# Kernel optimization log

Hardware: AMD Instinct MI355X
Metric: run time of the kernel (lower is better)

The kernel has to match this reference:

```python
import math
import jax, jax.numpy as jnp
import numpy as np

DRAGON_ITERATIONS = 12
DRAGON_SMOOTHING = 0.1


def _dragon_patterns(iterations=DRAGON_ITERATIONS, smoothing=DRAGON_SMOOTHING):
    """Deterministic (non-learned) Dragon curve patterns, matching torch impl."""
    patterns = [np.array([0.5], dtype=np.float32)]
    kernel = np.ones(3, dtype=np.float32) / 3.0
    for _ in range(1, iterations):
        prev = patterns[-1]
        n = len(prev)
        newp = np.zeros(2 * n + 1, dtype=np.float32)
        newp[:n] = prev
        newp[n] = 0.5
        newp[n + 1:] = 1.0 - prev[::-1]
        if smoothing > 0:
            # conv1d with kernel_size=3, padding=1 (zero pad) == np.convolve 'same'
            newp = np.convolve(newp, kernel, mode='same').astype(np.float32)
        newp = (newp - newp.min()) / (newp.max() - newp.min() + 1e-8)
        patterns.append(newp.astype(np.float32))
    return patterns

_PATTERNS = _dragon_patterns()


def _interp_pattern(seq_len):
    """Linearly interpolate selected dragon pattern to seq_len (static shapes)."""
    it = min(int(math.log2(seq_len)), DRAGON_ITERATIONS - 1)
    pattern = _PATTERNS[it]
    if len(pattern) == seq_len:
        w = pattern.copy()
    else:
        x_old = np.linspace(0.0, 1.0, len(pattern), dtype=np.float64)
        x_new = np.linspace(0.0, 1.0, seq_len, dtype=np.float64)
        w = np.interp(x_new, x_old, pattern.astype(np.float64)).astype(np.float32)
    return it, jnp.asarray(w)


def setup_inputs() -> dict:
    key = jax.random.key(0)
    ks = jax.random.split(key, 8)
    B, S, D = 8, 2048, 512
    query = jax.random.normal(ks[0], (B, S, D), dtype=jnp.float32)
    k = jax.random.normal(ks[1], (B, S, D), dtype=jnp.float32)
    value = jax.random.normal(ks[2], (B, S, D), dtype=jnp.float32)
    pattern_scale = jnp.ones((DRAGON_ITERATIONS,), dtype=jnp.float32)
    pattern_bias = jnp.zeros((DRAGON_ITERATIONS,), dtype=jnp.float32)
    w1 = jax.random.normal(ks[3], (DRAGON_ITERATIONS, 64), dtype=jnp.float32) * (1.0 / math.sqrt(DRAGON_ITERATIONS))
    b1 = jnp.zeros((64,), dtype=jnp.float32)
    w2 = jax.random.normal(ks[4], (64, 1), dtype=jnp.float32) * (1.0 / 8.0)
    b2 = jnp.zeros((1,), dtype=jnp.float32)
    return {"query": query, "key": k, "value": value,
            "pattern_scale": pattern_scale, "pattern_bias": pattern_bias,
            "w1": w1, "b1": b1, "w2": w2, "b2": b2}


def reference(query, key, value, pattern_scale, pattern_bias, w1, b1, w2, b2):
    B, S, D = key.shape
    it, base_w = _interp_pattern(S)
    # learned affine + softplus on dragon weights
    dragon_w = jax.nn.softplus(base_w * pattern_scale[it] + pattern_bias[it])  # [S]
    weighted_keys = key * dragon_w[None, :, None]                              # [B,S,D]
    scores = jnp.einsum('bqd,bkd->bqk', query, weighted_keys) / math.sqrt(D)   # [B,S,S]
    attn = jax.nn.softmax(scores, axis=-1)
    # blend factor from one-hot iteration features through tiny MLP
    feat = jax.nn.one_hot(it, DRAGON_ITERATIONS, dtype=query.dtype)            # [12]
    h = jax.nn.relu(feat @ w1 + b1)
    blend = jax.nn.sigmoid(h @ w2 + b2)                                        # [1]
    blend = blend[0]
    final_attn = blend * attn + (1.0 - blend) / S                              # uniform blend
    out = jnp.einsum('bqk,bkd->bqd', final_attn, value)                        # [B,S,D]
    # original does output.squeeze(1); S>1 so it's a no-op here
    return out
```

## Files before the change

### kernel.cpp

```cpp
#include <hip/hip_runtime.h>
#include <cstdint>

#define DEV __device__ __forceinline__

typedef float f32x4 __attribute__((ext_vector_type(4)));
typedef short s16x8 __attribute__((ext_vector_type(8)));

DEV unsigned short f2bf(float f){
    unsigned u = __builtin_bit_cast(unsigned, f);
    u = u + 0x7fffu + ((u >> 16) & 1u);
    return (unsigned short)(u >> 16);
}
DEV float bf2f(unsigned short h){
    unsigned u = ((unsigned)h) << 16;
    return __builtin_bit_cast(float, u);
}

typedef const void __attribute__((address_space(1)))* gcp;
typedef void __attribute__((address_space(3)))* lp;
DEV void gload_lds16(const void* g, void* l){
    __builtin_amdgcn_global_load_lds((gcp)g, (lp)l, 16, 0, 0);
}

__global__ __launch_bounds__(256) void k_prep(
    const float* __restrict__ scale, const float* __restrict__ bias,
    const float* __restrict__ w1, const float* __restrict__ b1,
    const float* __restrict__ w2, const float* __restrict__ b2,
    float* __restrict__ dragon_w, float* __restrict__ blend_out)
{
    __shared__ float A[4095];
    __shared__ float Bb[4095];
    __shared__ float red[8];
    int tid = threadIdx.x;
    int lane = tid & 63, w = tid >> 6;

    if (tid == 0) A[0] = 0.5f;
    __syncthreads();
    float lo = 0.f, rden = 1.f;
    int len = 1;
    const float third = 1.0f/3.0f;
    for (int it = 1; it < 12; ++it){
        int n = len, nl = 2*n + 1;
        for (int i = tid; i < nl; i += 256){
            float v;
            if (i < n)       v = (A[i] - lo) * rden;
            else if (i == n) v = 0.5f;
            else             v = 1.0f - (A[2*n - i] - lo) * rden;
            Bb[i] = v;
        }
        __syncthreads();
        float mn = 3.4e38f, mx = -3.4e38f;
        for (int i = tid; i < nl; i += 256){
            float s = Bb[i];
            if (i > 0)    s += Bb[i-1];
            if (i < nl-1) s += Bb[i+1];
            s *= third;
            A[i] = s;
            mn = fminf(mn, s); mx = fmaxf(mx, s);
        }
        #pragma unroll
        for (int off = 32; off > 0; off >>= 1){
            mn = fminf(mn, __shfl_xor(mn, off, 64));
            mx = fmaxf(mx, __shfl_xor(mx, off, 64));
        }
        if (lane == 0){ red[w] = mn; red[4 + w] = mx; }
        __syncthreads();
        mn = fminf(fminf(red[0], red[1]), fminf(red[2], red[3]));
        mx = fmaxf(fmaxf(red[4], red[5]), fmaxf(red[6], red[7]));
        lo = mn; rden = 1.0f / (mx - mn + 1e-8f);
        len = nl;
        __syncthreads();
    }
    float sc = scale[11], bi = bias[11];
    for (int i = tid; i < 2048; i += 256){
        float x = (A[2*i] - lo) * rden * sc + bi;
        dragon_w[i] = fmaxf(x, 0.f) + log1pf(__expf(-fabsf(x)));
    }
    if (tid < 64){
        float h = fmaxf(w1[11*64 + tid] + b1[tid], 0.f);
        float c = h * w2[tid];
        for (int off = 32; off > 0; off >>= 1) c += __shfl_xor(c, off, 64);
        if (tid == 0) blend_out[0] = 1.f/(1.f + __expf(-(c + b2[0])));
    }
}

__global__ __launch_bounds__(256) void k_conv(
    const float* __restrict__ Q, const float* __restrict__ K,
    const float* __restrict__ V, const float* __restrict__ dragon_w,
    unsigned short* __restrict__ Qb, unsigned short* __restrict__ Kb,
    unsigned short* __restrict__ Vt, float* __restrict__ vmean_part)
{
    __shared__ float sh[4480];
    int tid = threadIdx.x;
    int bx  = blockIdx.x;

    if (bx < 1024){
        const long long total4 = (long long)8*2048*512/4;
        long long stride = 1024LL*256;
        for (long long i = (long long)bx*256 + tid; i < total4; i += stride){
            long long base = i*4;
            int s = (int)((base >> 9) & 2047);
            float wv = dragon_w[s];
            const float4 q = *(const float4*)(Q + base);
            const float4 k = *(const float4*)(K + base);
            ushort4 qo, ko;
            qo.x = f2bf(q.x);    qo.y = f2bf(q.y);    qo.z = f2bf(q.z);    qo.w = f2bf(q.w);
            ko.x = f2bf(k.x*wv); ko.y = f2bf(k.y*wv); ko.z = f2bf(k.z*wv); ko.w = f2bf(k.w*wv);
            *(ushort4*)(Qb + base) = qo;
            *(ushort4*)(Kb + base) = ko;
        }
        return;
    }

    int t = bx - 1024;
    int stile = t & 31, dtile = (t >> 5) & 7, b = t >> 8;
    int s0 = stile*64, d0 = dtile*64;
    float (*tile)[66] = (float(*)[66])sh;
    float* red = sh + 4224;
    int tx = tid & 63, ty = tid >> 6;
    const float* src = V + ((long long)b*2048 + s0)*512 + d0;
    #pragma unroll
    for (int r = 0; r < 16; ++r){
        int row = r*4 + ty;
        tile[row][tx] = src[(long long)row*512 + tx];
    }
    __syncthreads();
    unsigned short* dst = Vt + ((long long)b*512 + d0)*2048 + s0;
    #pragma unroll
    for (int r = 0; r < 16; ++r){
        int drow = r*4 + ty;
        dst[(long long)drow*2048 + tx] = f2bf(tile[tx][drow]);
    }
    int dcol = tid & 63, sp = tid >> 6;
    float s = 0.f;
    #pragma unroll
    for (int ii = 0; ii < 16; ++ii) s += tile[sp*16 + ii][dcol];
    red[sp*64 + dcol] = s;
    __syncthreads();
    if (sp == 0){
        float tot = red[dcol] + red[64+dcol] + red[128+dcol] + red[192+dcol];
        vmean_part[stile*4096 + b*512 + d0 + dcol] = tot * (1.0f/2048.0f);
    }
}

#define SCALE_QK 0.04419417382415922f

__global__ __launch_bounds__(256) void k_gemm_qk(
    const unsigned short* __restrict__ Qb, const unsigned short* __restrict__ Kb,
    const float* __restrict__ vmean_part, float* __restrict__ vmean,
    unsigned short* __restrict__ Sp)
{
    __shared__ unsigned short At[128*64];
    __shared__ unsigned short Bt[128*64];
    int tid = threadIdx.x;
    int lane = tid & 63, wave = tid >> 6;
    int wm = wave >> 1, wn = wave & 1;
    int ln = lane & 15, q4 = lane >> 4;
    int sx = ln & 7;
    int q0 = blockIdx.y*128, k0 = blockIdx.x*128, b = blockIdx.z;

    if (blockIdx.x == 0 && blockIdx.y == 0){
        #pragma unroll
        for (int rep = 0; rep < 2; ++rep){
            int idx = b*512 + rep*256 + tid;
            float s = 0.f;
            #pragma unroll
            for (int st = 0; st < 32; ++st) s += vmean_part[st*4096 + idx];
            vmean[idx] = s;
        }
    }

    const unsigned short* Abase = Qb + ((long long)b*2048 + q0)*512;
    const unsigned short* Bbase = Kb + ((long long)b*2048 + k0)*512;

    f32x4 acc[4][4];
    #pragma unroll
    for (int i = 0; i < 4; ++i)
        #pragma unroll
        for (int j = 0; j < 4; ++j) acc[i][j] = (f32x4)0.0f;

    int cc = lane & 7;
    int rg = lane >> 3;
    for (int kt = 0; kt < 8; ++kt){
        #pragma unroll
        for (int c = 0; c < 4; ++c){
            int chunk = wave*4 + c;
            int row = chunk*8 + rg;
            int gc  = cc ^ (row & 7);
            gload_lds16(Abase + (long long)row*512 + kt*64 + gc*8, &At[chunk*512]);
            gload_lds16(Bbase + (long long)row*512 + kt*64 + gc*8, &Bt[chunk*512]);
        }
        __syncthreads();
        #pragma unroll
        for (int ks = 0; ks < 2; ++ks){
            s16x8 af[4], bfr[4];
            int cs = ((ks*4 + q4) ^ sx) * 8;
            #pragma unroll
            for (int i = 0; i < 4; ++i)
                af[i] = *(const s16x8*)&At[(wm*64 + i*16 + ln)*64 + cs];
            #pragma unroll
            for (int j = 0; j < 4; ++j)
                bfr[j] = *(const s16x8*)&Bt[(wn*64 + j*16 + ln)*64 + cs];
            #pragma unroll
            for (int i = 0; i < 4; ++i)
                #pragma unroll
                for (int j = 0; j < 4; ++j)
                    acc[i][j] = __builtin_amdgcn_mfma_f32_16x16x32_bf16(af[i], bfr[j], acc[i][j], 0, 0, 0);
        }
        __syncthreads();
    }
    unsigned short* outp = Sp + (long long)b*2048*2048;
    #pragma unroll
    for (int i = 0; i < 4; ++i){
        #pragma unroll
        for (int j = 0; j < 4; ++j){
            #pragma unroll
            for (int r = 0; r < 4; ++r){
                int q = q0 + wm*64 + i*16 + q4*4 + r;
                int k = k0 + wn*64 + j*16 + ln;
                float v = __expf(acc[i][j][r] * SCALE_QK);
                outp[(long long)q*2048 + k] = f2bf(v);
            }
        }
    }
}

__global__ __launch_bounds__(256) void k_gemm_pv(
    const unsigned short* __restrict__ Sp, const unsigned short* __restrict__ Vt,
    const float* __restrict__ vmean, const float* __restrict__ blendp,
    float* __restrict__ out)
{
    __shared__ unsigned short At[128*64];
    __shared__ unsigned short Bt[128*64];
    __shared__ float l_sh[128];
    int tid = threadIdx.x;
    int lane = tid & 63, wave = tid >> 6;
    int wm = wave >> 1, wn = wave & 1;
    int ln = lane & 15, q4 = lane >> 4;
    int sx = ln & 7;
    int q0 = blockIdx.y*128, d0 = blockIdx.x*128, b = blockIdx.z;
    const unsigned short* Abase = Sp + (long long)b*2048*2048 + (long long)q0*2048;
    const unsigned short* Bbase = Vt + ((long long)b*512 + d0)*2048;

    f32x4 acc[4][4];
    #pragma unroll
    for (int i = 0; i < 4; ++i)
        #pragma unroll
        for (int j = 0; j < 4; ++j) acc[i][j] = (f32x4)0.0f;
    float lsum[4] = {0.f, 0.f, 0.f, 0.f};

    int cc = lane & 7;
    int rg = lane >> 3;
    for (int kt = 0; kt < 32; ++kt){
        #pragma unroll
        for (int c = 0; c < 4; ++c){
            int chunk = wave*4 + c;
            int row = chunk*8 + rg;
            int gc  = cc ^ (row & 7);
            gload_lds16(Abase + (long long)row*2048 + kt*64 + gc*8, &At[chunk*512]);
            gload_lds16(Bbase + (long long)row*2048 + kt*64 + gc*8, &Bt[chunk*512]);
        }
        __syncthreads();
        #pragma unroll
        for (int ks = 0; ks < 2; ++ks){
            s16x8 af[4], bfr[4];
            int cs = ((ks*4 + q4) ^ sx) * 8;
            #pragma unroll
            for (int i = 0; i < 4; ++i)
                af[i] = *(const s16x8*)&At[(wm*64 + i*16 + ln)*64 + cs];
            #pragma unroll
            for (int j = 0; j < 4; ++j)
                bfr[j] = *(const s16x8*)&Bt[(wn*64 + j*16 + ln)*64 + cs];
            if (wn == 0){
                #pragma unroll
                for (int i = 0; i < 4; ++i){
                    float s = 0.f;
                    #pragma unroll
                    for (int jj = 0; jj < 8; ++jj) s += bf2f((unsigned short)af[i][jj]);
                    lsum[i] += s;
                }
            }
            #pragma unroll
            for (int i = 0; i < 4; ++i)
                #pragma unroll
                for (int j = 0; j < 4; ++j)
                    acc[i][j] = __builtin_amdgcn_mfma_f32_16x16x32_bf16(af[i], bfr[j], acc[i][j], 0, 0, 0);
        }
        __syncthreads();
    }
    if (wn == 0){
        #pragma unroll
        for (int i = 0; i < 4; ++i){
            float v = lsum[i];
            v += __shfl_xor(v, 16, 64);
            v += __shfl_xor(v, 32, 64);
            if (lane < 16) l_sh[wm*64 + i*16 + lane] = v;
        }
    }
    __syncthreads();

    float blend = blendp[0];
    float ib = 1.0f - blend;
    float* obase = out + ((long long)b*2048 + q0)*512 + d0;
    float vm[4];
    #pragma unroll
    for (int j = 0; j < 4; ++j) vm[j] = vmean[b*512 + d0 + wn*64 + j*16 + ln];
    #pragma unroll
    for (int i = 0; i < 4; ++i){
        #pragma unroll
        for (int r = 0; r < 4; ++r){
            int ql = wm*64 + i*16 + q4*4 + r;
            float linv = 1.0f / l_sh[ql];
            #pragma unroll
            for (int j = 0; j < 4; ++j){
                int dl = wn*64 + j*16 + ln;
                obase[(long long)ql*512 + dl] = blend*acc[i][j][r]*linv + ib*vm[j];
            }
        }
    }
}

extern "C" void kernel_launch(void* const* d_in, const int* in_sizes, int n_in,
                              void* d_out, int out_size, void* d_ws, size_t ws_size,
                              hipStream_t stream)
{
    (void)in_sizes; (void)n_in; (void)out_size; (void)ws_size;
    const float* Q  = (const float*)d_in[0];
    const float* K  = (const float*)d_in[1];
    const float* V  = (const float*)d_in[2];
    const float* ps = (const float*)d_in[3];
    const float* pb = (const float*)d_in[4];
    const float* w1 = (const float*)d_in[5];
    const float* b1 = (const float*)d_in[6];
    const float* w2 = (const float*)d_in[7];
    const float* b2 = (const float*)d_in[8];
    float* out = (float*)d_out;

    char* ws = (char*)d_ws;
    float* dragon_w        = (float*)(ws);
    float* blend           = (float*)(ws + 8192);
    float* vmean           = (float*)(ws + 16384);
    float* vmean_part      = (float*)(ws + 32768);
    size_t off = 32768 + (size_t)512*1024;
    unsigned short* Qb     = (unsigned short*)(ws + off);
    unsigned short* Kb     = (unsigned short*)(ws + off + (size_t)16*1024*1024);
    unsigned short* Vt     = (unsigned short*)(ws + off + (size_t)32*1024*1024);
    unsigned short* Sp     = (unsigned short*)(ws + off + (size_t)48*1024*1024);

    hipLaunchKernelGGL(k_prep,    dim3(1),         dim3(256), 0, stream,
                       ps, pb, w1, b1, w2, b2, dragon_w, blend);
    hipLaunchKernelGGL(k_conv,    dim3(3072),      dim3(256), 0, stream,
                       Q, K, V, dragon_w, Qb, Kb, Vt, vmean_part);
    hipLaunchKernelGGL(k_gemm_qk, dim3(16, 16, 8), dim3(256), 0, stream,
                       Qb, Kb, vmean_part, vmean, Sp);
    hipLaunchKernelGGL(k_gemm_pv, dim3(4, 16, 8),  dim3(256), 0, stream,
                       Sp, Vt, vmean, blend, out);
}
```

Before: 269.9 us.

## Fuse prep into conversion kernel, apply dragon weights in QK epilogue, widen QK tile

```diff
diff --git a/kernel.cpp b/kernel.cpp
--- a/kernel.cpp
+++ b/kernel.cpp
@@ -22,18 +22,75 @@
     __builtin_amdgcn_global_load_lds((gcp)g, (lp)l, 16, 0, 0);
 }
 
-__global__ __launch_bounds__(256) void k_prep(
+#define SCALE_QK 0.04419417382415922f
+
+__global__ __launch_bounds__(256) void k_conv(
+    const float* __restrict__ Q, const float* __restrict__ K,
+    const float* __restrict__ V,
     const float* __restrict__ scale, const float* __restrict__ bias,
     const float* __restrict__ w1, const float* __restrict__ b1,
     const float* __restrict__ w2, const float* __restrict__ b2,
-    float* __restrict__ dragon_w, float* __restrict__ blend_out)
+    unsigned short* __restrict__ Qb, unsigned short* __restrict__ Kb,
+    unsigned short* __restrict__ Vt, float* __restrict__ vmean,
+    float* __restrict__ dragon_wq, float* __restrict__ blend_out)
 {
-    __shared__ float A[4095];
-    __shared__ float Bb[4095];
-    __shared__ float red[8];
+    __shared__ float sh[8200];
     int tid = threadIdx.x;
+    int bx  = blockIdx.x;
+
+    if (bx < 1024){
+        const long long total4 = (long long)8*2048*512/4;
+        long long stride = 1024LL*256;
+        for (long long i = (long long)bx*256 + tid; i < total4; i += stride){
+            long long base = i*4;
+            const float4 q = *(const float4*)(Q + base);
+            const float4 k = *(const float4*)(K + base);
+            ushort4 qo, ko;
+            qo.x = f2bf(q.x); qo.y = f2bf(q.y); qo.z = f2bf(q.z); qo.w = f2bf(q.w);
+            ko.x = f2bf(k.x); ko.y = f2bf(k.y); ko.z = f2bf(k.z); ko.w = f2bf(k.w);
+            *(ushort4*)(Qb + base) = qo;
+            *(ushort4*)(Kb + base) = ko;
+        }
+        return;
+    }
+
+    if (bx < 3072){
+        int t = bx - 1024;
+        int stile = t & 31, dtile = (t >> 5) & 7, b = t >> 8;
+        int s0 = stile*64, d0 = dtile*64;
+        float (*tile)[66] = (float(*)[66])sh;
+        float* red = sh + 4224;
+        int tx = tid & 63, ty = tid >> 6;
+        const float* src = V + ((long long)b*2048 + s0)*512 + d0;
+        #pragma unroll
+        for (int r = 0; r < 16; ++r){
+            int row = r*4 + ty;
+            tile[row][tx] = src[(long long)row*512 + tx];
+        }
+        __syncthreads();
+        unsigned short* dst = Vt + ((long long)b*512 + d0)*2048 + s0;
+        #pragma unroll
+        for (int r = 0; r < 16; ++r){
+            int drow = r*4 + ty;
+            dst[(long long)drow*2048 + tx] = f2bf(tile[tx][drow]);
+        }
+        int dcol = tid & 63, sp = tid >> 6;
+        float s = 0.f;
+        #pragma unroll
+        for (int ii = 0; ii < 16; ++ii) s += tile[sp*16 + ii][dcol];
+        red[sp*64 + dcol] = s;
+        __syncthreads();
+        if (sp == 0){
+            float tot = red[dcol] + red[64+dcol] + red[128+dcol] + red[192+dcol];
+            atomicAdd(&vmean[b*512 + d0 + dcol], tot * (1.0f/2048.0f));
+        }
+        return;
+    }
+
+    float* A    = sh;
+    float* Bb   = sh + 4095;
+    float* red8 = sh + 8190;
     int lane = tid & 63, w = tid >> 6;
-
     if (tid == 0) A[0] = 0.5f;
     __syncthreads();
     float lo = 0.f, rden = 1.f;
@@ -63,10 +120,10 @@
             mn = fminf(mn, __shfl_xor(mn, off, 64));
             mx = fmaxf(mx, __shfl_xor(mx, off, 64));
         }
-        if (lane == 0){ red[w] = mn; red[4 + w] = mx; }
-        __syncthreads();
-        mn = fminf(fminf(red[0], red[1]), fminf(red[2], red[3]));
-        mx = fmaxf(fmaxf(red[4], red[5]), fmaxf(red[6], red[7]));
+        if (lane == 0){ red8[w] = mn; red8[4 + w] = mx; }
+        __syncthreads();
+        mn = fminf(fminf(red8[0], red8[1]), fminf(red8[2], red8[3]));
+        mx = fmaxf(fmaxf(red8[4], red8[5]), fmaxf(red8[6], red8[7]));
         lo = mn; rden = 1.0f / (mx - mn + 1e-8f);
         len = nl;
         __syncthreads();
@@ -74,7 +131,7 @@
     float sc = scale[11], bi = bias[11];
     for (int i = tid; i < 2048; i += 256){
         float x = (A[2*i] - lo) * rden * sc + bi;
-        dragon_w[i] = fmaxf(x, 0.f) + log1pf(__expf(-fabsf(x)));
+        dragon_wq[i] = (fmaxf(x, 0.f) + log1pf(__expf(-fabsf(x)))) * SCALE_QK;
     }
     if (tid < 64){
         float h = fmaxf(w1[11*64 + tid] + b1[tid], 0.f);
@@ -84,103 +141,28 @@
     }
 }
 
-__global__ __launch_bounds__(256) void k_conv(
-    const float* __restrict__ Q, const float* __restrict__ K,
-    const float* __restrict__ V, const float* __restrict__ dragon_w,
-    unsigned short* __restrict__ Qb, unsigned short* __restrict__ Kb,
-    unsigned short* __restrict__ Vt, float* __restrict__ vmean_part)
-{
-    __shared__ float sh[4480];
-    int tid = threadIdx.x;
-    int bx  = blockIdx.x;
-
-    if (bx < 1024){
-        const long long total4 = (long long)8*2048*512/4;
-        long long stride = 1024LL*256;
-        for (long long i = (long long)bx*256 + tid; i < total4; i += stride){
-            long long base = i*4;
-            int s = (int)((base >> 9) & 2047);
-            float wv = dragon_w[s];
-            const float4 q = *(const float4*)(Q + base);
-            const float4 k = *(const float4*)(K + base);
-            ushort4 qo, ko;
-            qo.x = f2bf(q.x);    qo.y = f2bf(q.y);    qo.z = f2bf(q.z);    qo.w = f2bf(q.w);
-            ko.x = f2bf(k.x*wv); ko.y = f2bf(k.y*wv); ko.z = f2bf(k.z*wv); ko.w = f2bf(k.w*wv);
-            *(ushort4*)(Qb + base) = qo;
-            *(ushort4*)(Kb + base) = ko;
-        }
-        return;
-    }
-
-    int t = bx - 1024;
-    int stile = t & 31, dtile = (t >> 5) & 7, b = t >> 8;
-    int s0 = stile*64, d0 = dtile*64;
-    float (*tile)[66] = (float(*)[66])sh;
-    float* red = sh + 4224;
-    int tx = tid & 63, ty = tid >> 6;
-    const float* src = V + ((long long)b*2048 + s0)*512 + d0;
-    #pragma unroll
-    for (int r = 0; r < 16; ++r){
-        int row = r*4 + ty;
-        tile[row][tx] = src[(long long)row*512 + tx];
-    }
-    __syncthreads();
-    unsigned short* dst = Vt + ((long long)b*512 + d0)*2048 + s0;
-    #pragma unroll
-    for (int r = 0; r < 16; ++r){
-        int drow = r*4 + ty;
-        dst[(long long)drow*2048 + tx] = f2bf(tile[tx][drow]);
-    }
-    int dcol = tid & 63, sp = tid >> 6;
-    float s = 0.f;
-    #pragma unroll
-    for (int ii = 0; ii < 16; ++ii) s += tile[sp*16 + ii][dcol];
-    red[sp*64 + dcol] = s;
-    __syncthreads();
-    if (sp == 0){
-        float tot = red[dcol] + red[64+dcol] + red[128+dcol] + red[192+dcol];
-        vmean_part[stile*4096 + b*512 + d0 + dcol] = tot * (1.0f/2048.0f);
-    }
-}
-
-#define SCALE_QK 0.04419417382415922f
-
 __global__ __launch_bounds__(256) void k_gemm_qk(
     const unsigned short* __restrict__ Qb, const unsigned short* __restrict__ Kb,
-    const float* __restrict__ vmean_part, float* __restrict__ vmean,
-    unsigned short* __restrict__ Sp)
+    const float* __restrict__ dragon_wq, unsigned short* __restrict__ Sp)
 {
     __shared__ unsigned short At[128*64];
-    __shared__ unsigned short Bt[128*64];
+    __shared__ unsigned short Bt[256*64];
     int tid = threadIdx.x;
     int lane = tid & 63, wave = tid >> 6;
     int wm = wave >> 1, wn = wave & 1;
     int ln = lane & 15, q4 = lane >> 4;
     int sx = ln & 7;
-    int q0 = blockIdx.y*128, k0 = blockIdx.x*128, b = blockIdx.z;
-
-    if (blockIdx.x == 0 && blockIdx.y == 0){
-        #pragma unroll
-        for (int rep = 0; rep < 2; ++rep){
-            int idx = b*512 + rep*256 + tid;
-            float s = 0.f;
-            #pragma unroll
-            for (int st = 0; st < 32; ++st) s += vmean_part[st*4096 + idx];
-            vmean[idx] = s;
-        }
-    }
-
+    int q0 = blockIdx.y*128, k0 = blockIdx.x*256, b = blockIdx.z;
     const unsigned short* Abase = Qb + ((long long)b*2048 + q0)*512;
     const unsigned short* Bbase = Kb + ((long long)b*2048 + k0)*512;
 
-    f32x4 acc[4][4];
+    f32x4 acc[4][8];
     #pragma unroll
     for (int i = 0; i < 4; ++i)
         #pragma unroll
-        for (int j = 0; j < 4; ++j) acc[i][j] = (f32x4)0.0f;
-
-    int cc = lane & 7;
-    int rg = lane >> 3;
+        for (int j = 0; j < 8; ++j) acc[i][j] = (f32x4)0.0f;
+
+    int cc = lane & 7, rg = lane >> 3;
     for (int kt = 0; kt < 8; ++kt){
         #pragma unroll
         for (int c = 0; c < 4; ++c){
@@ -188,38 +170,46 @@
             int row = chunk*8 + rg;
             int gc  = cc ^ (row & 7);
             gload_lds16(Abase + (long long)row*512 + kt*64 + gc*8, &At[chunk*512]);
+        }
+        #pragma unroll
+        for (int c = 0; c < 8; ++c){
+            int chunk = wave*8 + c;
+            int row = chunk*8 + rg;
+            int gc  = cc ^ (row & 7);
             gload_lds16(Bbase + (long long)row*512 + kt*64 + gc*8, &Bt[chunk*512]);
         }
         __syncthreads();
         #pragma unroll
         for (int ks = 0; ks < 2; ++ks){
-            s16x8 af[4], bfr[4];
             int cs = ((ks*4 + q4) ^ sx) * 8;
+            s16x8 af[4], bfr[8];
             #pragma unroll
             for (int i = 0; i < 4; ++i)
                 af[i] = *(const s16x8*)&At[(wm*64 + i*16 + ln)*64 + cs];
             #pragma unroll
-            for (int j = 0; j < 4; ++j)
-                bfr[j] = *(const s16x8*)&Bt[(wn*64 + j*16 + ln)*64 + cs];
+            for (int j = 0; j < 8; ++j)
+                bfr[j] = *(const s16x8*)&Bt[(wn*128 + j*16 + ln)*64 + cs];
             #pragma unroll
             for (int i = 0; i < 4; ++i)
                 #pragma unroll
-                for (int j = 0; j < 4; ++j)
+                for (int j = 0; j < 8; ++j)
                     acc[i][j] = __builtin_amdgcn_mfma_f32_16x16x32_bf16(af[i], bfr[j], acc[i][j], 0, 0, 0);
         }
         __syncthreads();
     }
+    float wq[8];
+    #pragma unroll
+    for (int j = 0; j < 8; ++j) wq[j] = dragon_wq[k0 + wn*128 + j*16 + ln];
     unsigned short* outp = Sp + (long long)b*2048*2048;
     #pragma unroll
     for (int i = 0; i < 4; ++i){
         #pragma unroll
-        for (int j = 0; j < 4; ++j){
+        for (int j = 0; j < 8; ++j){
             #pragma unroll
             for (int r = 0; r < 4; ++r){
                 int q = q0 + wm*64 + i*16 + q4*4 + r;
-                int k = k0 + wn*64 + j*16 + ln;
-                float v = __expf(acc[i][j][r] * SCALE_QK);
-                outp[(long long)q*2048 + k] = f2bf(v);
+                int k = k0 + wn*128 + j*16 + ln;
+                outp[(long long)q*2048 + k] = f2bf(__expf(acc[i][j][r] * wq[j]));
             }
         }
     }
@@ -249,8 +239,7 @@
         for (int j = 0; j < 4; ++j) acc[i][j] = (f32x4)0.0f;
     float lsum[4] = {0.f, 0.f, 0.f, 0.f};
 
-    int cc = lane & 7;
-    int rg = lane >> 3;
+    int cc = lane & 7, rg = lane >> 3;
     for (int kt = 0; kt < 32; ++kt){
         #pragma unroll
         for (int c = 0; c < 4; ++c){
@@ -263,8 +252,8 @@
         __syncthreads();
         #pragma unroll
         for (int ks = 0; ks < 2; ++ks){
+            int cs = ((ks*4 + q4) ^ sx) * 8;
             s16x8 af[4], bfr[4];
-            int cs = ((ks*4 + q4) ^ sx) * 8;
             #pragma unroll
             for (int i = 0; i < 4; ++i)
                 af[i] = *(const s16x8*)&At[(wm*64 + i*16 + ln)*64 + cs];
@@ -337,22 +326,20 @@
     float* out = (float*)d_out;
 
     char* ws = (char*)d_ws;
-    float* dragon_w        = (float*)(ws);
+    float* dragon_wq       = (float*)(ws);
     float* blend           = (float*)(ws + 8192);
     float* vmean           = (float*)(ws + 16384);
-    float* vmean_part      = (float*)(ws + 32768);
-    size_t off = 32768 + (size_t)512*1024;
+    size_t off = 32768;
     unsigned short* Qb     = (unsigned short*)(ws + off);
     unsigned short* Kb     = (unsigned short*)(ws + off + (size_t)16*1024*1024);
     unsigned short* Vt     = (unsigned short*)(ws + off + (size_t)32*1024*1024);
     unsigned short* Sp     = (unsigned short*)(ws + off + (size_t)48*1024*1024);
 
-    hipLaunchKernelGGL(k_prep,    dim3(1),         dim3(256), 0, stream,
-                       ps, pb, w1, b1, w2, b2, dragon_w, blend);
-    hipLaunchKernelGGL(k_conv,    dim3(3072),      dim3(256), 0, stream,
-                       Q, K, V, dragon_w, Qb, Kb, Vt, vmean_part);
-    hipLaunchKernelGGL(k_gemm_qk, dim3(16, 16, 8), dim3(256), 0, stream,
-                       Qb, Kb, vmean_part, vmean, Sp);
+    hipMemsetAsync(vmean, 0, 4096*sizeof(float), stream);
+    hipLaunchKernelGGL(k_conv,    dim3(3073),      dim3(256), 0, stream,
+                       Q, K, V, ps, pb, w1, b1, w2, b2, Qb, Kb, Vt, vmean, dragon_wq, blend);
+    hipLaunchKernelGGL(k_gemm_qk, dim3(8, 16, 8),  dim3(256), 0, stream,
+                       Qb, Kb, dragon_wq, Sp);
     hipLaunchKernelGGL(k_gemm_pv, dim3(4, 16, 8),  dim3(256), 0, stream,
                        Sp, Vt, vmean, blend, out);
 }
```

Result: slower. 291.4 us (+8.0%).
